# Performance work log

Measured on AMD Instinct MI355X. Metric: run time of the kernel, lower is better.

The kernel has to match this reference:

```python
import jax, jax.numpy as jnp
import numpy as np

B, S, H = 2, 2048, 1024
E, K, F = 8, 2, 4096


def setup_inputs() -> dict:
    key = jax.random.key(0)
    ks = jax.random.split(key, 7)
    s_h = 1.0 / np.sqrt(H)
    s_f = 1.0 / np.sqrt(F)
    return {
        "hidden_states": jax.random.normal(ks[0], (B, S, H), jnp.float32),
        "Wr": jax.random.normal(ks[1], (H, E), jnp.float32) * s_h,
        "br": jnp.zeros((E,), jnp.float32),
        "W1": jax.random.normal(ks[2], (E, H, F), jnp.float32) * s_h,
        "b1": jnp.zeros((E, F), jnp.float32),
        "W2": jax.random.normal(ks[3], (E, F, H), jnp.float32) * s_f,
        "b2": jnp.zeros((E, H), jnp.float32),
    }


def _moe_forward(hidden_states, Wr, br, W1, b1, W2, b2):
    b, s, h = hidden_states.shape
    x = hidden_states.reshape(-1, h)  # [T, H]
    # --- router: top-k over softmax probs, renormalized ---
    logits = x @ Wr + br  # [T, E]
    probs = jax.nn.softmax(logits, axis=-1)
    top_w, top_i = jax.lax.top_k(probs, K)  # [T, K]
    weights = top_w / jnp.sum(top_w, axis=-1, keepdims=True)  # [T, K]
    # --- dense-equivalent expert dispatch + combine ---
    # per-token per-expert combine weight (zero for unselected experts)
    out = jnp.zeros_like(x)
    for e in range(E):
        w_e = jnp.sum(weights * (top_i == e), axis=-1)  # [T]
        h_e = jax.nn.gelu(x @ W1[e] + b1[e], approximate=False)  # [T, F]
        y_e = h_e @ W2[e] + b2[e]  # [T, H]
        out = out + w_e[:, None] * y_e
    # --- aux load-balance loss (counts are constants wrt grads) ---
    counts = jnp.sum(jax.nn.one_hot(top_i, E, dtype=logits.dtype), axis=(0, 1))  # [E]
    load = counts / (top_i.size)
    aux_loss = jnp.mean((load - 1.0 / E) ** 2)
    # --- z-loss ---
    z_loss = jnp.mean(jax.nn.logsumexp(logits, axis=-1))
    total_loss = 0.01 * aux_loss + 0.001 * z_loss
    return out.reshape(b, s, h), total_loss


def reference(hidden_states, Wr, br, W1, b1, W2, b2):
    output, total_loss = _moe_forward(hidden_states, Wr, br, W1, b1, W2, b2)
    return output, total_loss
```

## Files before the change

### kernel.cpp

```cpp
#include <hip/hip_runtime.h>
#include <stdint.h>
#include <math.h>

#define T_TOK 4096
#define H_DIM 1024
#define E_EXP 8
#define F_DIM 4096
#define NASSIGN (T_TOK * 2)
#define OUT_ELEMS ((size_t)T_TOK * H_DIM)
#define YB_ELEMS ((size_t)8192 * H_DIM)
#define TL 257

typedef unsigned short u16;
typedef __attribute__((ext_vector_type(8))) short short8;
typedef __attribute__((ext_vector_type(4))) short short4v;
typedef __attribute__((ext_vector_type(4))) float f32x4;

__device__ __forceinline__ u16 f2bf(float f) {
  union { float f; uint32_t u; } c; c.f = f;
  uint32_t u = c.u;
  return (u16)((u + 0x7FFFu + ((u >> 16) & 1u)) >> 16);
}

__device__ __forceinline__ float fast_erf(float u) {
  const float au = fabsf(u);
  const float t = __builtin_amdgcn_rcpf(__builtin_fmaf(0.3275911f, au, 1.0f));
  float p = __builtin_fmaf(1.061405429f, t, -1.453152027f);
  p = __builtin_fmaf(p, t, 1.421413741f);
  p = __builtin_fmaf(p, t, -0.284496736f);
  p = __builtin_fmaf(p, t, 0.254829592f);
  p = p * t;
  const float y = __builtin_fmaf(-p, __expf(-au * au), 1.0f);
  return copysignf(y, u);
}

__device__ __forceinline__ void gl_lds16(const void* g, void* l) {
  __builtin_amdgcn_global_load_lds(
      (const __attribute__((address_space(1))) uint32_t*)g,
      (__attribute__((address_space(3))) uint32_t*)(uintptr_t)l, 16, 0, 0);
}

__device__ __forceinline__ void transpose_strip(
    const float* __restrict__ in, u16* __restrict__ out, int R, int C,
    int bx , int by , int bz, u16* tile) {
  const size_t eoff = (size_t)bz * R * C;
  const int wave = threadIdx.x >> 6, lane = threadIdx.x & 63;
  const float* inp = in + eoff + ((size_t)by * 64) * C + bx * 256;
#pragma unroll
  for (int p = 0; p < 16; ++p) {
    const int r = p * 4 + wave;
    const float4 v = *(const float4*)(inp + (size_t)r * C + lane * 4);
    u16* trow = tile + r * TL + lane * 4;
    trow[0] = f2bf(v.x); trow[1] = f2bf(v.y); trow[2] = f2bf(v.z); trow[3] = f2bf(v.w);
  }
  __syncthreads();
  const int cl = threadIdx.x >> 3;
  const int rg = (threadIdx.x & 7) * 8;
#pragma unroll
  for (int tx = 0; tx < 4; ++tx) {
    u16* op = out + (((size_t)bz * (C >> 6) + bx * 4 + tx) * (R >> 6) + by) * 4096;
#pragma unroll
    for (int p = 0; p < 2; ++p) {
      const int c = cl + p * 32;
      short8 o;
#pragma unroll
      for (int j = 0; j < 8; ++j) o[j] = (short)tile[(rg + j) * TL + tx * 64 + c];
      *(short8*)(op + c * 64 + rg) = o;
    }
  }
}

__global__ __launch_bounds__(256) void prep_kernel(
    const float* __restrict__ x, const float* __restrict__ Wr,
    const float* __restrict__ br, u16* __restrict__ xb,
    int* __restrict__ tki, float* __restrict__ tkw,
    int* __restrict__ counts, float* __restrict__ zsum,
    const float* __restrict__ W1, u16* __restrict__ w1t) {
  __shared__ u16 tile[64 * TL];
  __shared__ int lcnt[8];
  __shared__ float lzv[16];
  const int id = blockIdx.x;

  if (id >= 256) {
    const int q = id - 256;
    transpose_strip(W1, w1t, H_DIM, F_DIM, q & 15, (q >> 4) & 15, q >> 8, tile);
    return;
  }

  const int wave = threadIdx.x >> 6;
  const int lane = threadIdx.x & 63;
  if (threadIdx.x < 8) lcnt[threadIdx.x] = 0;
  __syncthreads();
#pragma unroll
  for (int it = 0; it < 4; ++it) {
    const int t = id * 16 + wave * 4 + it;
    const float* xr = x + (size_t)t * H_DIM;
    u16* xbr = xb + (size_t)t * H_DIM;
    float acc[8];
#pragma unroll
    for (int e = 0; e < 8; ++e) acc[e] = 0.0f;
#pragma unroll
    for (int j = 0; j < 4; ++j) {
      const int h0 = j * 256 + lane * 4;
      const float4 xv = *(const float4*)(xr + h0);
      const float vv[4] = {xv.x, xv.y, xv.z, xv.w};
      short4v pk;
#pragma unroll
      for (int i = 0; i < 4; ++i) {
        pk[i] = (short)f2bf(vv[i]);
        const float4 w0 = *(const float4*)(Wr + (size_t)(h0 + i) * 8);
        const float4 w1 = *(const float4*)(Wr + (size_t)(h0 + i) * 8 + 4);
        acc[0] += vv[i] * w0.x; acc[1] += vv[i] * w0.y;
        acc[2] += vv[i] * w0.z; acc[3] += vv[i] * w0.w;
        acc[4] += vv[i] * w1.x; acc[5] += vv[i] * w1.y;
        acc[6] += vv[i] * w1.z; acc[7] += vv[i] * w1.w;
      }
      *(short4v*)(xbr + h0) = pk;
    }
#pragma unroll
    for (int e = 0; e < 8; ++e) {
      float v = acc[e];
#pragma unroll
      for (int s = 32; s > 0; s >>= 1) v += __shfl_xor(v, s);
      acc[e] = v;
    }
    if (lane == 0) {
      float l[8];
#pragma unroll
      for (int e = 0; e < 8; ++e) l[e] = acc[e] + br[e];
      float mx = l[0];
#pragma unroll
      for (int e = 1; e < 8; ++e) mx = fmaxf(mx, l[e]);
      float p[8], s = 0.0f;
#pragma unroll
      for (int e = 0; e < 8; ++e) { p[e] = __expf(l[e] - mx); s += p[e]; }
      int i0 = 0;
#pragma unroll
      for (int e = 1; e < 8; ++e) if (p[e] > p[i0]) i0 = e;
      int i1 = (i0 == 0) ? 1 : 0;
#pragma unroll
      for (int e = 0; e < 8; ++e) if (e != i1 && e != i0 && p[e] > p[i1]) i1 = e;
      const float ws = p[i0] + p[i1];
      tki[2 * t] = i0; tki[2 * t + 1] = i1;
      tkw[2 * t] = p[i0] / ws; tkw[2 * t + 1] = p[i1] / ws;
      atomicAdd(&lcnt[i0], 1);
      atomicAdd(&lcnt[i1], 1);
      lzv[wave * 4 + it] = mx + logf(s);
    }
  }
  __syncthreads();
  if (threadIdx.x < 8) {
    const int c = lcnt[threadIdx.x];
    if (c) atomicAdd(&counts[threadIdx.x], c);
  }
  if (threadIdx.x == 64) {
    float zs = 0.0f;
#pragma unroll
    for (int i = 0; i < 16; ++i) zs += lzv[i];
    atomicAdd(zsum, zs);
  }
}

__global__ void scatter_kernel(const int* __restrict__ tki, const float* __restrict__ tkw,
                               const int* __restrict__ counts, int* __restrict__ cursor,
                               int* __restrict__ perm, float* __restrict__ pw,
                               int* __restrict__ islot,
                               const float* __restrict__ zsum, float* __restrict__ out_loss) {
  int offs[8];
  {
    int a = 0;
#pragma unroll
    for (int e = 0; e < 8; ++e) { offs[e] = a; a += counts[e]; }
  }
  const int lane = threadIdx.x & 63;
  const int t = blockIdx.x * 256 + threadIdx.x;
#pragma unroll
  for (int k = 0; k < 2; ++k) {
    const int e = tki[2 * t + k];
    int slot = 0;
#pragma unroll
    for (int ee = 0; ee < 8; ++ee) {
      const unsigned long long mask = __ballot(e == ee);
      if (mask) {
        const int leader = __ffsll(mask) - 1;
        int b = 0;
        if (lane == leader) b = atomicAdd(&cursor[ee], (int)__popcll(mask));
        b = __shfl(b, leader);
        if (e == ee) {
          const int r = (int)__popcll(mask & ((1ull << lane) - 1ull));
          slot = offs[ee] + b + r;
        }
      }
    }
    perm[slot] = t;
    pw[slot] = tkw[2 * t + k];
    islot[2 * t + k] = slot;
  }
  if (blockIdx.x == 0 && threadIdx.x == 0) {
    float aux = 0.0f;
#pragma unroll
    for (int e = 0; e < 8; ++e) {
      const float d = (float)counts[e] / (float)NASSIGN - 0.125f;
      aux += d * d;
    }
    aux *= (1.0f / 8.0f);
    out_loss[0] = 0.01f * aux + 0.001f * (zsum[0] / (float)T_TOK);
  }
}


__global__ __launch_bounds__(256, 2) void gemm1_kernel(
    const u16* __restrict__ xb, const u16* __restrict__ w1t,
    const float* __restrict__ b1, const int* __restrict__ perm,
    const int* __restrict__ cnts, u16* __restrict__ hbuf,
    const float* __restrict__ W2, u16* __restrict__ w2t) {
  __shared__ __align__(16) u16 smem[24576];
  const int id = blockIdx.x;

  if (id >= 4096) {
    const int q = id - 4096;
    transpose_strip(W2, w2t, F_DIM, H_DIM, q & 3, (q >> 2) & 63, q >> 8, smem);
    return;
  }

  u16* As = smem;
  u16* Bs = smem + 16384;

  const int e = id & 7;
  const int wq = id >> 3;
  const int n0 = (wq & 31) << 7;
  const int m0 = (wq >> 5) << 8;
  int cnt, off;
  {
    int a = 0, c = 0;
#pragma unroll
    for (int i = 0; i < 8; ++i) { const int ci = cnts[i]; if (i < e) a += ci; if (i == e) c = ci; }
    cnt = c; off = a;
  }
  if (m0 >= cnt) return;

  const int tid = threadIdx.x;
  const int rbase = tid >> 3;
  const int kc = ((tid & 7) ^ (rbase & 7)) * 8;

  const u16* ap[8];
#pragma unroll
  for (int l = 0; l < 8; ++l) {
    int ra = m0 + rbase + l * 32; if (ra > cnt - 1) ra = cnt - 1;
    ap[l] = xb + (size_t)perm[off + ra] * H_DIM + kc;
  }
  const u16* bp0 = w1t + ((((size_t)e * (F_DIM >> 6) + (n0 >> 6)) * (H_DIM >> 6)) << 12)
                 + rbase * 64 + kc;
  const size_t bnt = (size_t)(H_DIM >> 6) << 12;

  const int wave = tid >> 6, lane = tid & 63;
  const int wm = (wave >> 1) * 128, wn = (wave & 1) * 64;
  const int lr = lane & 15, q = lane >> 4;
  const int qs0 = q ^ (lr & 7), qs1 = (4 + q) ^ (lr & 7);

  f32x4 acc[8][4];
#pragma unroll
  for (int i = 0; i < 8; ++i)
#pragma unroll
    for (int j = 0; j < 4; ++j) acc[i][j] = (f32x4)0.0f;

  const short8* Afr = (const short8*)As;
  const short8* Bfr = (const short8*)Bs;

  for (int k0 = 0; k0 < (H_DIM >> 6); ++k0) {
#pragma unroll
    for (int l = 0; l < 8; ++l) {
      gl_lds16(ap[l], &As[(size_t)(tid + l * 256) * 8]);
      ap[l] += 64;
    }
    gl_lds16(bp0,              &Bs[(size_t)tid * 8]);
    gl_lds16(bp0 + 2048,       &Bs[(size_t)(tid + 256) * 8]);
    gl_lds16(bp0 + bnt,        &Bs[(size_t)(tid + 512) * 8]);
    gl_lds16(bp0 + bnt + 2048, &Bs[(size_t)(tid + 768) * 8]);
    bp0 += 4096;
    __syncthreads();
#pragma unroll
    for (int s = 0; s < 2; ++s) {
      const int qs = s ? qs1 : qs0;
      short8 a[8], b[4];
#pragma unroll
      for (int i = 0; i < 8; ++i) a[i] = Afr[(wm + i * 16 + lr) * 8 + qs];
#pragma unroll
      for (int j = 0; j < 4; ++j) b[j] = Bfr[(wn + j * 16 + lr) * 8 + qs];
#pragma unroll
      for (int i = 0; i < 8; ++i)
#pragma unroll
        for (int j = 0; j < 4; ++j)
          acc[i][j] = __builtin_amdgcn_mfma_f32_16x16x32_bf16(a[i], b[j], acc[i][j], 0, 0, 0);
    }
    __syncthreads();
  }

#pragma unroll
  for (int h = 0; h < 2; ++h) {
    if ((wave >> 1) == h) {
#pragma unroll
      for (int i = 0; i < 8; ++i) {
#pragma unroll
        for (int rr = 0; rr < 4; ++rr) {
          const int rloc = i * 16 + q * 4 + rr;
#pragma unroll
          for (int j = 0; j < 4; ++j) {
            const int col = wn + j * 16 + lr;
            const float v = acc[i][j][rr] + b1[e * F_DIM + n0 + col];
            const float g = 0.5f * v * (1.0f + fast_erf(v * 0.70710678118654752f));
            smem[(rloc << 7) + (col ^ (q << 4))] = f2bf(g);
          }
        }
      }
    }
    __syncthreads();
#pragma unroll
    for (int p = 0; p < 8; ++p) {
      const int ml = p * 16 + (tid >> 4);
      const int nl = (tid & 15) * 8;
      const int m = m0 + h * 128 + ml;
      if (m < cnt) {
        const int qq = (ml >> 2) & 3;
        *(short8*)(hbuf + (size_t)(off + m) * F_DIM + n0 + nl) =
            *(const short8*)(smem + (ml << 7) + (nl ^ (qq << 4)));
      }
    }
    __syncthreads();
  }
}

__global__ __launch_bounds__(256, 2) void gemm2_kernel(
    const u16* __restrict__ hbuf, const u16* __restrict__ w2t,
    const float* __restrict__ b2, const float* __restrict__ pw,
    const int* __restrict__ cnts, float* __restrict__ ybuf) {
  const int id = blockIdx.x;
  const int e = id & 7;
  const int wq = id >> 3;
  const int n0 = (wq & 7) << 7;
  const int ks = (wq >> 3) & 1;
  const int m0 = (wq >> 4) << 8;
  int cnt, off;
  {
    int a = 0, c = 0;
#pragma unroll
    for (int i = 0; i < 8; ++i) { const int ci = cnts[i]; if (i < e) a += ci; if (i == e) c = ci; }
    cnt = c; off = a;
  }
  if (m0 >= cnt) return;

  __shared__ __align__(16) u16 smem[24576];
  u16* As = smem;
  u16* Bs = smem + 16384;

  const int tid = threadIdx.x;
  const int rbase = tid >> 3;
  const int kc = ((tid & 7) ^ (rbase & 7)) * 8;

  const u16* ap[8];
#pragma unroll
  for (int l = 0; l < 8; ++l) {
    int ra = m0 + rbase + l * 32; if (ra > cnt - 1) ra = cnt - 1;
    ap[l] = hbuf + (size_t)(off + ra) * F_DIM + (ks << 11) + kc;
  }
  const u16* bp0 = w2t + ((((size_t)e * (H_DIM >> 6) + (n0 >> 6)) * (F_DIM >> 6)) << 12)
                 + ((size_t)(ks << 5) << 12) + rbase * 64 + kc;
  const size_t bnt = (size_t)(F_DIM >> 6) << 12;

  const int wave = tid >> 6, lane = tid & 63;
  const int wm = (wave >> 1) * 128, wn = (wave & 1) * 64;
  const int lr = lane & 15, q = lane >> 4;
  const int qs0 = q ^ (lr & 7), qs1 = (4 + q) ^ (lr & 7);

  f32x4 acc[8][4];
#pragma unroll
  for (int i = 0; i < 8; ++i)
#pragma unroll
    for (int j = 0; j < 4; ++j) acc[i][j] = (f32x4)0.0f;

  const short8* Afr = (const short8*)As;
  const short8* Bfr = (const short8*)Bs;

  for (int k0 = 0; k0 < 32; ++k0) {
#pragma unroll
    for (int l = 0; l < 8; ++l) {
      gl_lds16(ap[l], &As[(size_t)(tid + l * 256) * 8]);
      ap[l] += 64;
    }
    gl_lds16(bp0,              &Bs[(size_t)tid * 8]);
    gl_lds16(bp0 + 2048,       &Bs[(size_t)(tid + 256) * 8]);
    gl_lds16(bp0 + bnt,        &Bs[(size_t)(tid + 512) * 8]);
    gl_lds16(bp0 + bnt + 2048, &Bs[(size_t)(tid + 768) * 8]);
    bp0 += 4096;
    __syncthreads();
#pragma unroll
    for (int s = 0; s < 2; ++s) {
      const int qs = s ? qs1 : qs0;
      short8 a[8], b[4];
#pragma unroll
      for (int i = 0; i < 8; ++i) a[i] = Afr[(wm + i * 16 + lr) * 8 + qs];
#pragma unroll
      for (int j = 0; j < 4; ++j) b[j] = Bfr[(wn + j * 16 + lr) * 8 + qs];
#pragma unroll
      for (int i = 0; i < 8; ++i)
#pragma unroll
        for (int j = 0; j < 4; ++j)
          acc[i][j] = __builtin_amdgcn_mfma_f32_16x16x32_bf16(a[i], b[j], acc[i][j], 0, 0, 0);
    }
    __syncthreads();
  }

  float* yb = ybuf + (size_t)ks * YB_ELEMS;
#pragma unroll
  for (int i = 0; i < 8; ++i) {
#pragma unroll
    for (int rr = 0; rr < 4; ++rr) {
      const int m = m0 + wm + i * 16 + q * 4 + rr;
      if (m < cnt) {
        const int slot = off + m;
        const float w = pw[slot];
        float* orow = yb + (size_t)slot * H_DIM;
#pragma unroll
        for (int j = 0; j < 4; ++j) {
          const int col = n0 + wn + j * 16 + lr;
          float y = acc[i][j][rr];
          if (ks == 0) y += b2[e * H_DIM + col];
          orow[col] = w * y;
        }
      }
    }
  }
}

__global__ __launch_bounds__(256) void combine_kernel(
    const float* __restrict__ ybuf, const int* __restrict__ islot,
    float* __restrict__ out) {
  const int t = blockIdx.x;
  const int s0 = islot[2 * t];
  const int s1 = islot[2 * t + 1];
  const int c = threadIdx.x * 4;
  const float4 a0 = *(const float4*)(ybuf + (size_t)s0 * H_DIM + c);
  const float4 a1 = *(const float4*)(ybuf + YB_ELEMS + (size_t)s0 * H_DIM + c);
  const float4 b0 = *(const float4*)(ybuf + (size_t)s1 * H_DIM + c);
  const float4 b1 = *(const float4*)(ybuf + YB_ELEMS + (size_t)s1 * H_DIM + c);
  float4 r;
  r.x = a0.x + a1.x + b0.x + b1.x;
  r.y = a0.y + a1.y + b0.y + b1.y;
  r.z = a0.z + a1.z + b0.z + b1.z;
  r.w = a0.w + a1.w + b0.w + b1.w;
  *(float4*)(out + (size_t)t * H_DIM + c) = r;
}


extern "C" void kernel_launch(void* const* d_in, const int* in_sizes, int n_in,
                              void* d_out, int out_size, void* d_ws, size_t ws_size,
                              hipStream_t stream) {
  const float* x  = (const float*)d_in[0];
  const float* Wr = (const float*)d_in[1];
  const float* br = (const float*)d_in[2];
  const float* W1 = (const float*)d_in[3];
  const float* b1 = (const float*)d_in[4];
  const float* W2 = (const float*)d_in[5];
  const float* b2 = (const float*)d_in[6];
  float* out = (float*)d_out;

  char* ws = (char*)d_ws;
  u16* xb    = (u16*)(ws);
  u16* w1t   = (u16*)(ws + 8388608ull);
  u16* w2t   = (u16*)(ws + 75497472ull);
  u16* hbuf  = (u16*)(ws + 142606336ull);
  float* ybuf = (float*)(ws + 8388608ull);
  int*   tki    = (int*)(ws + 209715200ull);
  float* tkw    = (float*)(ws + 209747968ull);
  int*   perm   = (int*)(ws + 209780736ull);
  float* pw     = (float*)(ws + 209813504ull);
  int*   counts = (int*)(ws + 209846272ull);
  int*   cursor = counts + 8;
  float* zsum   = (float*)(counts + 16);
  int*   islot  = (int*)(ws + 209846400ull);

  hipMemsetAsync(counts, 0, 128, stream);

  prep_kernel<<<2304, 256, 0, stream>>>(x, Wr, br, xb, tki, tkw, counts, zsum, W1, w1t);
  scatter_kernel<<<T_TOK / 256, 256, 0, stream>>>(tki, tkw, counts, cursor, perm, pw,
                                                  islot, zsum, out + OUT_ELEMS);
  gemm1_kernel<<<6144, 256, 0, stream>>>(xb, w1t, b1, perm, counts, hbuf, W2, w2t);
  gemm2_kernel<<<2048, 256, 0, stream>>>(hbuf, w2t, b2, pw, counts, ybuf);
  combine_kernel<<<T_TOK, 256, 0, stream>>>(ybuf, islot, out);
}
```

Measured before the change: 571.4 us.

## Double-buffer expert GEMMs with 512-thread 256x256 tiles and phased MFMA scheduling

```diff
diff --git a/kernel.cpp b/kernel.cpp
--- a/kernel.cpp
+++ b/kernel.cpp
@@ -42,7 +42,7 @@
 
 __device__ __forceinline__ void transpose_strip(
     const float* __restrict__ in, u16* __restrict__ out, int R, int C,
-    int bx , int by , int bz, u16* tile) {
+    int bx, int by, int bz, u16* tile) {
   const size_t eoff = (size_t)bz * R * C;
   const int wave = threadIdx.x >> 6, lane = threadIdx.x & 63;
   const float* inp = in + eoff + ((size_t)by * 64) * C + bx * 256;
@@ -67,6 +67,32 @@
       for (int j = 0; j < 8; ++j) o[j] = (short)tile[(rg + j) * TL + tx * 64 + c];
       *(short8*)(op + c * 64 + rg) = o;
     }
+  }
+}
+
+__device__ __forceinline__ void transpose_strip512(
+    const float* __restrict__ in, u16* __restrict__ out, int R, int C,
+    int bx, int by, int bz, u16* tile) {
+  const size_t eoff = (size_t)bz * R * C;
+  const int wv = threadIdx.x >> 6, lane = threadIdx.x & 63;
+  const float* inp = in + eoff + ((size_t)by * 64) * C + bx * 256;
+#pragma unroll
+  for (int p = 0; p < 8; ++p) {
+    const int r = p * 8 + wv;
+    const float4 v = *(const float4*)(inp + (size_t)r * C + lane * 4);
+    u16* trow = tile + r * TL + lane * 4;
+    trow[0] = f2bf(v.x); trow[1] = f2bf(v.y); trow[2] = f2bf(v.z); trow[3] = f2bf(v.w);
+  }
+  __syncthreads();
+  const int c = threadIdx.x >> 3;
+  const int rg = (threadIdx.x & 7) * 8;
+#pragma unroll
+  for (int tx = 0; tx < 4; ++tx) {
+    u16* op = out + (((size_t)bz * (C >> 6) + bx * 4 + tx) * (R >> 6) + by) * 4096;
+    short8 o;
+#pragma unroll
+    for (int j = 0; j < 8; ++j) o[j] = (short)tile[(rg + j) * TL + tx * 64 + c];
+    *(short8*)(op + c * 64 + rg) = o;
   }
 }
 
@@ -209,136 +235,91 @@
 }
 
 
-__global__ __launch_bounds__(256, 2) void gemm1_kernel(
+#define G_STAGE_A(NB)                                                        \
+  { _Pragma("unroll")                                                        \
+    for (int l = 0; l < 4; ++l) {                                            \
+      gl_lds16(ap[l], &smem[(NB) + l * 4096 + tid * 8]); ap[l] += 64;        \
+    } }
+
+#define G_STAGE_B(NB)                                                        \
+  { _Pragma("unroll")                                                        \
+    for (int l = 0; l < 4; ++l) {                                            \
+      gl_lds16(bp[l], &smem[32768 + (NB) + l * 4096 + tid * 8]); bp[l] += 4096; \
+    } }
+
+#define PH_BARRIER                                                           \
+  asm volatile("" ::: "memory");                                             \
+  __builtin_amdgcn_s_barrier();                                              \
+  asm volatile("" ::: "memory");
+
+#define MFMA_J(J)                                                            \
+  { _Pragma("unroll")                                                        \
+    for (int i = 0; i < 8; ++i) {                                            \
+      acc[i][J] = __builtin_amdgcn_mfma_f32_16x16x32_bf16(a0[i], bj0, acc[i][J], 0, 0, 0); \
+      acc[i][J] = __builtin_amdgcn_mfma_f32_16x16x32_bf16(a1[i], bj1, acc[i][J], 0, 0, 0); \
+    } }
+
+#define KLOOP(NKT)                                                           \
+  for (int kt = 0; kt < (NKT); ++kt) {                                       \
+    const int cb = (kt & 1) << 14;                                           \
+    const int nb = 16384 - cb;                                               \
+    const short8* Afr = (const short8*)(smem + cb);                          \
+    const short8* Bfr = (const short8*)(smem + 32768 + cb);                  \
+    asm volatile("s_waitcnt vmcnt(0)" ::: "memory");                         \
+    __builtin_amdgcn_sched_barrier(0);                                       \
+    __builtin_amdgcn_s_barrier();                                            \
+    asm volatile("" ::: "memory");                                           \
+    short8 a0[8], a1[8], bj0, bj1;                                           \
+    _Pragma("unroll")                                                        \
+    for (int i = 0; i < 8; ++i) {                                            \
+      a0[i] = Afr[(wm + i * 16 + lr) * 8 + qs0];                             \
+      a1[i] = Afr[(wm + i * 16 + lr) * 8 + qs1];                             \
+    }                                                                        \
+    bj0 = Bfr[(wn + lr) * 8 + qs0];                                          \
+    bj1 = Bfr[(wn + lr) * 8 + qs1];                                          \
+    if (kt + 1 < (NKT)) { G_STAGE_A(nb) }                                    \
+    __builtin_amdgcn_s_setprio(1);                                           \
+    MFMA_J(0)                                                                \
+    __builtin_amdgcn_s_setprio(0);                                           \
+    PH_BARRIER                                                               \
+    bj0 = Bfr[(wn + 16 + lr) * 8 + qs0];                                     \
+    bj1 = Bfr[(wn + 16 + lr) * 8 + qs1];                                     \
+    if (kt + 1 < (NKT)) { G_STAGE_B(nb) }                                    \
+    __builtin_amdgcn_s_setprio(1);                                           \
+    MFMA_J(1)                                                                \
+    __builtin_amdgcn_s_setprio(0);                                           \
+    PH_BARRIER                                                               \
+    bj0 = Bfr[(wn + 32 + lr) * 8 + qs0];                                     \
+    bj1 = Bfr[(wn + 32 + lr) * 8 + qs1];                                     \
+    __builtin_amdgcn_s_setprio(1);                                           \
+    MFMA_J(2)                                                                \
+    __builtin_amdgcn_s_setprio(0);                                           \
+    PH_BARRIER                                                               \
+    bj0 = Bfr[(wn + 48 + lr) * 8 + qs0];                                     \
+    bj1 = Bfr[(wn + 48 + lr) * 8 + qs1];                                     \
+    __builtin_amdgcn_s_setprio(1);                                           \
+    MFMA_J(3)                                                                \
+    __builtin_amdgcn_s_setprio(0);                                           \
+    PH_BARRIER                                                               \
+  }
+
+__global__ __launch_bounds__(512, 2) void gemm1_kernel(
     const u16* __restrict__ xb, const u16* __restrict__ w1t,
     const float* __restrict__ b1, const int* __restrict__ perm,
     const int* __restrict__ cnts, u16* __restrict__ hbuf,
     const float* __restrict__ W2, u16* __restrict__ w2t) {
-  __shared__ __align__(16) u16 smem[24576];
+  __shared__ __align__(16) u16 smem[65536];
   const int id = blockIdx.x;
 
-  if (id >= 4096) {
-    const int q = id - 4096;
-    transpose_strip(W2, w2t, F_DIM, H_DIM, q & 3, (q >> 2) & 63, q >> 8, smem);
+  if (id >= 2048) {
+    const int q = id - 2048;
+    transpose_strip512(W2, w2t, F_DIM, H_DIM, q & 3, (q >> 2) & 63, q >> 8, smem);
     return;
   }
-
-  u16* As = smem;
-  u16* Bs = smem + 16384;
 
   const int e = id & 7;
   const int wq = id >> 3;
-  const int n0 = (wq & 31) << 7;
-  const int m0 = (wq >> 5) << 8;
-  int cnt, off;
-  {
-    int a = 0, c = 0;
-#pragma unroll
-    for (int i = 0; i < 8; ++i) { const int ci = cnts[i]; if (i < e) a += ci; if (i == e) c = ci; }
-    cnt = c; off = a;
-  }
-  if (m0 >= cnt) return;
-
-  const int tid = threadIdx.x;
-  const int rbase = tid >> 3;
-  const int kc = ((tid & 7) ^ (rbase & 7)) * 8;
-
-  const u16* ap[8];
-#pragma unroll
-  for (int l = 0; l < 8; ++l) {
-    int ra = m0 + rbase + l * 32; if (ra > cnt - 1) ra = cnt - 1;
-    ap[l] = xb + (size_t)perm[off + ra] * H_DIM + kc;
-  }
-  const u16* bp0 = w1t + ((((size_t)e * (F_DIM >> 6) + (n0 >> 6)) * (H_DIM >> 6)) << 12)
-                 + rbase * 64 + kc;
-  const size_t bnt = (size_t)(H_DIM >> 6) << 12;
-
-  const int wave = tid >> 6, lane = tid & 63;
-  const int wm = (wave >> 1) * 128, wn = (wave & 1) * 64;
-  const int lr = lane & 15, q = lane >> 4;
-  const int qs0 = q ^ (lr & 7), qs1 = (4 + q) ^ (lr & 7);
-
-  f32x4 acc[8][4];
-#pragma unroll
-  for (int i = 0; i < 8; ++i)
-#pragma unroll
-    for (int j = 0; j < 4; ++j) acc[i][j] = (f32x4)0.0f;
-
-  const short8* Afr = (const short8*)As;
-  const short8* Bfr = (const short8*)Bs;
-
-  for (int k0 = 0; k0 < (H_DIM >> 6); ++k0) {
-#pragma unroll
-    for (int l = 0; l < 8; ++l) {
-      gl_lds16(ap[l], &As[(size_t)(tid + l * 256) * 8]);
-      ap[l] += 64;
-    }
-    gl_lds16(bp0,              &Bs[(size_t)tid * 8]);
-    gl_lds16(bp0 + 2048,       &Bs[(size_t)(tid + 256) * 8]);
-    gl_lds16(bp0 + bnt,        &Bs[(size_t)(tid + 512) * 8]);
-    gl_lds16(bp0 + bnt + 2048, &Bs[(size_t)(tid + 768) * 8]);
-    bp0 += 4096;
-    __syncthreads();
-#pragma unroll
-    for (int s = 0; s < 2; ++s) {
-      const int qs = s ? qs1 : qs0;
-      short8 a[8], b[4];
-#pragma unroll
-      for (int i = 0; i < 8; ++i) a[i] = Afr[(wm + i * 16 + lr) * 8 + qs];
-#pragma unroll
-      for (int j = 0; j < 4; ++j) b[j] = Bfr[(wn + j * 16 + lr) * 8 + qs];
-#pragma unroll
-      for (int i = 0; i < 8; ++i)
-#pragma unroll
-        for (int j = 0; j < 4; ++j)
-          acc[i][j] = __builtin_amdgcn_mfma_f32_16x16x32_bf16(a[i], b[j], acc[i][j], 0, 0, 0);
-    }
-    __syncthreads();
-  }
-
-#pragma unroll
-  for (int h = 0; h < 2; ++h) {
-    if ((wave >> 1) == h) {
-#pragma unroll
-      for (int i = 0; i < 8; ++i) {
-#pragma unroll
-        for (int rr = 0; rr < 4; ++rr) {
-          const int rloc = i * 16 + q * 4 + rr;
-#pragma unroll
-          for (int j = 0; j < 4; ++j) {
-            const int col = wn + j * 16 + lr;
-            const float v = acc[i][j][rr] + b1[e * F_DIM + n0 + col];
-            const float g = 0.5f * v * (1.0f + fast_erf(v * 0.70710678118654752f));
-            smem[(rloc << 7) + (col ^ (q << 4))] = f2bf(g);
-          }
-        }
-      }
-    }
-    __syncthreads();
-#pragma unroll
-    for (int p = 0; p < 8; ++p) {
-      const int ml = p * 16 + (tid >> 4);
-      const int nl = (tid & 15) * 8;
-      const int m = m0 + h * 128 + ml;
-      if (m < cnt) {
-        const int qq = (ml >> 2) & 3;
-        *(short8*)(hbuf + (size_t)(off + m) * F_DIM + n0 + nl) =
-            *(const short8*)(smem + (ml << 7) + (nl ^ (qq << 4)));
-      }
-    }
-    __syncthreads();
-  }
-}
-
-__global__ __launch_bounds__(256, 2) void gemm2_kernel(
-    const u16* __restrict__ hbuf, const u16* __restrict__ w2t,
-    const float* __restrict__ b2, const float* __restrict__ pw,
-    const int* __restrict__ cnts, float* __restrict__ ybuf) {
-  const int id = blockIdx.x;
-  const int e = id & 7;
-  const int wq = id >> 3;
-  const int n0 = (wq & 7) << 7;
-  const int ks = (wq >> 3) & 1;
+  const int n0 = (wq & 15) << 8;
   const int m0 = (wq >> 4) << 8;
   int cnt, off;
   {
@@ -349,26 +330,24 @@
   }
   if (m0 >= cnt) return;
 
-  __shared__ __align__(16) u16 smem[24576];
-  u16* As = smem;
-  u16* Bs = smem + 16384;
-
   const int tid = threadIdx.x;
   const int rbase = tid >> 3;
   const int kc = ((tid & 7) ^ (rbase & 7)) * 8;
 
-  const u16* ap[8];
-#pragma unroll
-  for (int l = 0; l < 8; ++l) {
-    int ra = m0 + rbase + l * 32; if (ra > cnt - 1) ra = cnt - 1;
-    ap[l] = hbuf + (size_t)(off + ra) * F_DIM + (ks << 11) + kc;
-  }
-  const u16* bp0 = w2t + ((((size_t)e * (H_DIM >> 6) + (n0 >> 6)) * (F_DIM >> 6)) << 12)
-                 + ((size_t)(ks << 5) << 12) + rbase * 64 + kc;
-  const size_t bnt = (size_t)(F_DIM >> 6) << 12;
+  const u16* ap[4];
+#pragma unroll
+  for (int l = 0; l < 4; ++l) {
+    int ra = m0 + rbase + l * 64; if (ra > cnt - 1) ra = cnt - 1;
+    ap[l] = xb + (size_t)perm[off + ra] * H_DIM + kc;
+  }
+  const u16* bp[4];
+#pragma unroll
+  for (int l = 0; l < 4; ++l)
+    bp[l] = w1t + (((size_t)e * (F_DIM >> 6) + (n0 >> 6) + l) * (H_DIM >> 6)) * 4096
+          + rbase * 64 + kc;
 
   const int wave = tid >> 6, lane = tid & 63;
-  const int wm = (wave >> 1) * 128, wn = (wave & 1) * 64;
+  const int wm = (wave >> 2) * 128, wn = (wave & 3) * 64;
   const int lr = lane & 15, q = lane >> 4;
   const int qs0 = q ^ (lr & 7), qs1 = (4 + q) ^ (lr & 7);
 
@@ -378,37 +357,90 @@
 #pragma unroll
     for (int j = 0; j < 4; ++j) acc[i][j] = (f32x4)0.0f;
 
-  const short8* Afr = (const short8*)As;
-  const short8* Bfr = (const short8*)Bs;
-
-  for (int k0 = 0; k0 < 32; ++k0) {
-#pragma unroll
-    for (int l = 0; l < 8; ++l) {
-      gl_lds16(ap[l], &As[(size_t)(tid + l * 256) * 8]);
-      ap[l] += 64;
-    }
-    gl_lds16(bp0,              &Bs[(size_t)tid * 8]);
-    gl_lds16(bp0 + 2048,       &Bs[(size_t)(tid + 256) * 8]);
-    gl_lds16(bp0 + bnt,        &Bs[(size_t)(tid + 512) * 8]);
-    gl_lds16(bp0 + bnt + 2048, &Bs[(size_t)(tid + 768) * 8]);
-    bp0 += 4096;
-    __syncthreads();
-#pragma unroll
-    for (int s = 0; s < 2; ++s) {
-      const int qs = s ? qs1 : qs0;
-      short8 a[8], b[4];
-#pragma unroll
-      for (int i = 0; i < 8; ++i) a[i] = Afr[(wm + i * 16 + lr) * 8 + qs];
-#pragma unroll
-      for (int j = 0; j < 4; ++j) b[j] = Bfr[(wn + j * 16 + lr) * 8 + qs];
-#pragma unroll
-      for (int i = 0; i < 8; ++i)
-#pragma unroll
-        for (int j = 0; j < 4; ++j)
-          acc[i][j] = __builtin_amdgcn_mfma_f32_16x16x32_bf16(a[i], b[j], acc[i][j], 0, 0, 0);
-    }
-    __syncthreads();
-  }
+  G_STAGE_A(0)
+  G_STAGE_B(0)
+
+  KLOOP(H_DIM >> 6)
+
+#pragma unroll
+  for (int i = 0; i < 8; ++i) {
+#pragma unroll
+    for (int rr = 0; rr < 4; ++rr) {
+      const int row = wm + i * 16 + q * 4 + rr;
+#pragma unroll
+      for (int j = 0; j < 4; ++j) {
+        const int col = wn + j * 16 + lr;
+        const float v = acc[i][j][rr] + b1[e * F_DIM + n0 + col];
+        const float g = 0.5f * v * (1.0f + fast_erf(v * 0.70710678118654752f));
+        smem[(row << 8) + (col ^ (q << 4))] = f2bf(g);
+      }
+    }
+  }
+  __syncthreads();
+#pragma unroll
+  for (int p = 0; p < 16; ++p) {
+    const int row = p * 16 + (tid >> 5);
+    const int nl = (tid & 31) * 8;
+    const int m = m0 + row;
+    if (m < cnt) {
+      const int qq = (row >> 2) & 3;
+      *(short8*)(hbuf + (size_t)(off + m) * F_DIM + n0 + nl) =
+          *(const short8*)(smem + (row << 8) + (nl ^ (qq << 4)));
+    }
+  }
+}
+
+__global__ __launch_bounds__(512, 2) void gemm2_kernel(
+    const u16* __restrict__ hbuf, const u16* __restrict__ w2t,
+    const float* __restrict__ b2, const float* __restrict__ pw,
+    const int* __restrict__ cnts, float* __restrict__ ybuf) {
+  __shared__ __align__(16) u16 smem[65536];
+  const int id = blockIdx.x;
+  const int e = id & 7;
+  const int wq = id >> 3;
+  const int n0 = (wq & 3) << 8;
+  const int ks = (wq >> 2) & 1;
+  const int m0 = (wq >> 3) << 8;
+  int cnt, off;
+  {
+    int a = 0, c = 0;
+#pragma unroll
+    for (int i = 0; i < 8; ++i) { const int ci = cnts[i]; if (i < e) a += ci; if (i == e) c = ci; }
+    cnt = c; off = a;
+  }
+  if (m0 >= cnt) return;
+
+  const int tid = threadIdx.x;
+  const int rbase = tid >> 3;
+  const int kc = ((tid & 7) ^ (rbase & 7)) * 8;
+
+  const u16* ap[4];
+#pragma unroll
+  for (int l = 0; l < 4; ++l) {
+    int ra = m0 + rbase + l * 64; if (ra > cnt - 1) ra = cnt - 1;
+    ap[l] = hbuf + (size_t)(off + ra) * F_DIM + (ks << 11) + kc;
+  }
+  const u16* bp[4];
+#pragma unroll
+  for (int l = 0; l < 4; ++l)
+    bp[l] = w2t + (((size_t)e * (H_DIM >> 6) + (n0 >> 6) + l) * (F_DIM >> 6)
+                   + (ks << 5)) * 4096 + rbase * 64 + kc;
+
+  const int wave = tid >> 6, lane = tid & 63;
+  const int wm = (wave >> 2) * 128, wn = (wave & 3) * 64;
+  const int lr = lane & 15, q = lane >> 4;
+  const int qs0 = q ^ (lr & 7), qs1 = (4 + q) ^ (lr & 7);
+
+  f32x4 acc[8][4];
+#pragma unroll
+  for (int i = 0; i < 8; ++i)
+#pragma unroll
+    for (int j = 0; j < 4; ++j) acc[i][j] = (f32x4)0.0f;
+
+  G_STAGE_A(0)
+  G_STAGE_B(0)
+
+  KLOOP(32)
 
   float* yb = ybuf + (size_t)ks * YB_ELEMS;
 #pragma unroll
@@ -484,7 +516,7 @@
   prep_kernel<<<2304, 256, 0, stream>>>(x, Wr, br, xb, tki, tkw, counts, zsum, W1, w1t);
   scatter_kernel<<<T_TOK / 256, 256, 0, stream>>>(tki, tkw, counts, cursor, perm, pw,
                                                   islot, zsum, out + OUT_ELEMS);
-  gemm1_kernel<<<6144, 256, 0, stream>>>(xb, w1t, b1, perm, counts, hbuf, W2, w2t);
-  gemm2_kernel<<<2048, 256, 0, stream>>>(hbuf, w2t, b2, pw, counts, ybuf);
+  gemm1_kernel<<<4096, 512, 0, stream>>>(xb, w1t, b1, perm, counts, hbuf, W2, w2t);
+  gemm2_kernel<<<1024, 512, 0, stream>>>(hbuf, w2t, b2, pw, counts, ybuf);
   combine_kernel<<<T_TOK, 256, 0, stream>>>(ybuf, islot, out);
 }
```

Result: faster. 547.5 us (-4.2%).
